# Optimization experiments

Measured on AMD Instinct MI355X. Metric: run time of the kernel, lower is better.

## Reference

```python
import jax, jax.numpy as jnp
import numpy as np

N_NODES = 100000
N_EDGES = 640000
NIN = 128
NOUT = 128


def setup_inputs() -> dict:
    key = jax.random.key(0)
    ks = jax.random.split(key, 10)
    scale = 1.0 / np.sqrt(NIN)
    x = jax.random.normal(ks[0], (N_NODES, NIN), dtype=jnp.float32)
    edge_index = jax.random.randint(ks[1], (2, N_EDGES), 0, N_NODES, dtype=jnp.int64)
    edge_attr = jnp.zeros((N_EDGES, 1), dtype=jnp.float32)
    Wk = jax.random.uniform(ks[2], (NIN, NOUT), jnp.float32, -scale, scale)
    bk = jax.random.uniform(ks[3], (NOUT,), jnp.float32, -scale, scale)
    Wq = jax.random.uniform(ks[4], (NIN, NOUT), jnp.float32, -scale, scale)
    bq = jax.random.uniform(ks[5], (NOUT,), jnp.float32, -scale, scale)
    Wv = jax.random.uniform(ks[6], (NIN, NOUT), jnp.float32, -scale, scale)
    bv = jax.random.uniform(ks[7], (NOUT,), jnp.float32, -scale, scale)
    Wskip = jax.random.uniform(ks[8], (NIN, NOUT), jnp.float32, -scale, scale)
    bias = jax.random.uniform(ks[9], (NOUT,), jnp.float32, -scale, scale)
    return {
        "x": x, "edge_index": edge_index, "edge_attr": edge_attr,
        "Wk": Wk, "bk": bk, "Wq": Wq, "bq": bq,
        "Wv": Wv, "bv": bv, "Wskip": Wskip, "bias": bias,
    }


def reference(x, edge_index, edge_attr, Wk, bk, Wq, bq, Wv, bv, Wskip, bias):
    # PyG ResGatedGraphConv: out_i = W_skip x_i + b + sum_{j->i} sigmoid(k_i + q_j) * v_j
    # k = lin_key(x) (applied to dst), q = lin_query(x) (src), v = lin_value(x) (src)
    src, dst = edge_index[0], edge_index[1]
    k = x @ Wk + bk            # [N, NOUT]
    q = x @ Wq + bq            # [N, NOUT]
    v = x @ Wv + bv            # [N, NOUT]
    eta = jax.nn.sigmoid(k[dst] + q[src])   # [E, NOUT] per-edge gate
    msg = eta * v[src]                       # [E, NOUT]
    agg = jax.ops.segment_sum(msg, dst, num_segments=x.shape[0])  # [N, NOUT]
    return agg + x @ Wskip + bias
```

## Files before the change

kernel.cpp:

```cpp
#include <hip/hip_runtime.h>
#include <hip/hip_bf16.h>

typedef __bf16 v4bf __attribute__((ext_vector_type(4)));
typedef __bf16 v8bf __attribute__((ext_vector_type(8)));
typedef float  v16f __attribute__((ext_vector_type(16)));
typedef float  f4v  __attribute__((ext_vector_type(4)));
typedef unsigned int u4v __attribute__((ext_vector_type(4)));

#define LOG2E 1.44269504088896340736f

__device__ __forceinline__ unsigned short f2bf(float f) {
    union { float f; unsigned int u; } a; a.f = f;
    unsigned int r = a.u + 0x7FFFu + ((a.u >> 16) & 1u);
    return (unsigned short)(r >> 16);
}

__device__ __forceinline__ void unpack8v(u4v w, float* f) {
    #pragma unroll
    for (int i = 0; i < 4; ++i) {
        f[2 * i]     = __uint_as_float(w[i] << 16);
        f[2 * i + 1] = __uint_as_float(w[i] & 0xFFFF0000u);
    }
}

__global__ __launch_bounds__(256) void prep_w_zero(
    const float* __restrict__ Wk, const float* __restrict__ Wq,
    const float* __restrict__ Wv, const float* __restrict__ Ws,
    unsigned short* __restrict__ Wt, int* __restrict__ deg, int N)
{
    int i = blockIdx.x * 256 + threadIdx.x;
    if (i < 65536) {
        int m = i >> 14;
        int r = i & 16383;
        int n = r >> 7, k = r & 127;
        const float* W = (m == 0) ? Wk : (m == 1) ? Wq : (m == 2) ? Wv : Ws;
        float scale = (m == 0) ? -LOG2E : (m == 1) ? LOG2E : 1.0f;
        Wt[i] = f2bf(W[k * 128 + n] * scale);
    }
    if (i < N) deg[i] = 0;
}

__global__ __launch_bounds__(1024, 4) void gemm_fused(
    const float* __restrict__ x, int N,
    const unsigned short* __restrict__ Wt,
    const float* __restrict__ bk, const float* __restrict__ bq,
    const float* __restrict__ bv, const float* __restrict__ bs,
    unsigned short* __restrict__ kws, unsigned short* __restrict__ qv,
    float* __restrict__ out,
    const int* __restrict__ ei, int E,
    int* __restrict__ deg, int* __restrict__ pos)
{
    for (int e = blockIdx.x * 1024 + threadIdx.x; e < E; e += 1024 * 1024) {
        pos[e] = atomicAdd(&deg[ei[E + e]], 1);
    }

    __shared__ __align__(16) unsigned short xs[32 * 132];
    const int t   = threadIdx.x;
    const int wid = t >> 6;
    const int m   = wid >> 2;
    const int ct  = wid & 3;
    const int l   = t & 63;
    const int col = ct * 32 + (l & 31);
    const int kb  = (l >> 5) * 8;

    v8bf b[8];
    {
        const unsigned short* wp = Wt + m * 16384 + col * 128 + kb;
        #pragma unroll
        for (int c = 0; c < 8; ++c) b[c] = *(const v8bf*)(wp + c * 16);
    }
    const float* bvec = (m == 0) ? bk : (m == 1) ? bq : (m == 2) ? bv : bs;
    const float bcol = bvec[col] * ((m == 0) ? -LOG2E : (m == 1) ? LOG2E : 1.0f);
    unsigned short* dst; int dstride;
    if (m == 0)      { dst = kws;      dstride = 128; }
    else if (m == 1) { dst = qv;       dstride = 256; }
    else             { dst = qv + 128; dstride = 256; }

    const int srow = t >> 5;
    const int sk4  = (t & 31) << 2;
    const int rowb = 4 * (l >> 5);

    const int ntiles = (N + 31) >> 5;
    int tile = blockIdx.x;
    if (tile >= ntiles) return;

    float4 stg = make_float4(0.f, 0.f, 0.f, 0.f);
    {
        int gr = tile * 32 + srow;
        if (gr < N) stg = *(const float4*)(x + (size_t)gr * 128 + sk4);
    }

    const unsigned short* ap = xs + (l & 31) * 132 + kb;

    while (true) {
        ushort4 pk;
        pk.x = f2bf(stg.x); pk.y = f2bf(stg.y);
        pk.z = f2bf(stg.z); pk.w = f2bf(stg.w);
        *(ushort4*)(xs + srow * 132 + sk4) = pk;
        __syncthreads();

        int next = tile + gridDim.x;
        if (next < ntiles) {
            int gr = next * 32 + srow;
            stg = (gr < N) ? *(const float4*)(x + (size_t)gr * 128 + sk4)
                           : make_float4(0.f, 0.f, 0.f, 0.f);
        }

        v16f acc = {};
        #pragma unroll
        for (int c = 0; c < 8; ++c) {
            v4bf a0 = *(const v4bf*)(ap + c * 16);
            v4bf a1 = *(const v4bf*)(ap + c * 16 + 4);
            v8bf a = __builtin_shufflevector(a0, a1, 0, 1, 2, 3, 4, 5, 6, 7);
            acc = __builtin_amdgcn_mfma_f32_32x32x16_bf16(a, b[c], acc, 0, 0, 0);
        }

        const int r0 = tile * 32 + rowb;
        if (m == 3) {
            #pragma unroll
            for (int reg = 0; reg < 16; ++reg) {
                int row = r0 + (reg & 3) + 8 * (reg >> 2);
                if (row < N) out[(size_t)row * 128 + col] = acc[reg] + bcol;
            }
        } else {
            #pragma unroll
            for (int reg = 0; reg < 16; ++reg) {
                int row = r0 + (reg & 3) + 8 * (reg >> 2);
                if (row < N) dst[(size_t)row * dstride + col] = f2bf(acc[reg] + bcol);
            }
        }

        tile = next;
        if (tile >= ntiles) break;
        __syncthreads();
    }
}


__global__ __launch_bounds__(256) void scan_chunks(
    const int* __restrict__ deg, int N, int* __restrict__ rowStart,
    int* __restrict__ chunkTot)
{
    __shared__ int sums[256];
    const int t = threadIdx.x;
    const int base = blockIdx.x * 1024 + t * 4;
    int d0 = 0, d1 = 0, d2 = 0, d3 = 0;
    if (base + 3 < N) {
        int4 dd = *(const int4*)(deg + base);
        d0 = dd.x; d1 = dd.y; d2 = dd.z; d3 = dd.w;
    } else {
        if (base + 0 < N) d0 = deg[base + 0];
        if (base + 1 < N) d1 = deg[base + 1];
        if (base + 2 < N) d2 = deg[base + 2];
        if (base + 3 < N) d3 = deg[base + 3];
    }
    int tot = d0 + d1 + d2 + d3;
    sums[t] = tot;
    __syncthreads();
    #pragma unroll
    for (int off = 1; off < 256; off <<= 1) {
        int v = (t >= off) ? sums[t - off] : 0;
        __syncthreads();
        sums[t] += v;
        __syncthreads();
    }
    int excl = sums[t] - tot;
    if (base + 0 < N) rowStart[base + 0] = excl;
    if (base + 1 < N) rowStart[base + 1] = excl + d0;
    if (base + 2 < N) rowStart[base + 2] = excl + d0 + d1;
    if (base + 3 < N) rowStart[base + 3] = excl + d0 + d1 + d2;
    if (t == 255) chunkTot[blockIdx.x] = sums[255];
}

__global__ __launch_bounds__(256) void add_offsets(
    int* __restrict__ rowStart, const int* __restrict__ chunkTot,
    int N, int nChunks)
{
    __shared__ int s[128];
    const int t = threadIdx.x;
    if (t < 128) s[t] = (t < nChunks) ? chunkTot[t] : 0;
    __syncthreads();
    #pragma unroll
    for (int off = 1; off < 128; off <<= 1) {
        int u = 0;
        if (t < 128 && t >= off) u = s[t - off];
        __syncthreads();
        if (t < 128) s[t] += u;
        __syncthreads();
    }
    const int coff = (blockIdx.x == 0) ? 0 : s[blockIdx.x - 1];
    const int base = blockIdx.x * 1024 + t * 4;
    if (base + 3 < N) {
        int4 r = *(const int4*)(rowStart + base);
        r.x += coff; r.y += coff; r.z += coff; r.w += coff;
        *(int4*)(rowStart + base) = r;
    } else {
        #pragma unroll
        for (int j = 0; j < 4; ++j) {
            if (base + j < N) rowStart[base + j] += coff;
        }
    }
}

__global__ __launch_bounds__(256) void fill_csr(
    const int* __restrict__ ei, int E,
    const int* __restrict__ rowStart, const int* __restrict__ pos,
    int* __restrict__ elist)
{
    int e = blockIdx.x * 256 + threadIdx.x;
    if (e >= E) return;
    elist[rowStart[ei[E + e]] + pos[e]] = ei[e];
}

__global__ __launch_bounds__(256, 4) void gather_agg(
    const int* __restrict__ rowStart, const int* __restrict__ deg,
    const int* __restrict__ elist,
    const unsigned short* __restrict__ kws,
    const unsigned short* __restrict__ qv,
    float* __restrict__ out, int N)
{
    const int grp = threadIdx.x >> 4;
    const int fo  = (threadIdx.x & 15) << 3;
    const int gstride = gridDim.x * 16;
    const unsigned short* qvb = qv + fo;

    for (int node = blockIdx.x * 16 + grp; node < N; node += gstride) {
        float* orow = out + (size_t)node * 128 + fo;
        f4v o0 = *(const f4v*)(orow);
        f4v o1 = *(const f4v*)(orow + 4);
        u4v kraw = *(const u4v*)(kws + (size_t)node * 128 + fo);
        const int p0 = rowStart[node];
        const int dg = deg[node];
        const int e  = p0 + dg;
        const int eL = e - 1;

        float nkf[8];
        unpack8v(kraw, nkf);
        float acc[8] = {};

        for (int base = p0; base < e; base += 4) {
            int idx[4];
            #pragma unroll
            for (int s = 0; s < 4; ++s) {
                int pp = base + s;
                idx[s] = elist[pp < e ? pp : eL];
            }
            u4v qr[4], vr[4];
            #pragma unroll
            for (int s = 0; s < 4; ++s) {
                const unsigned short* r = qvb + (idx[s] << 8);
                qr[s] = *(const u4v*)(r);
                vr[s] = *(const u4v*)(r + 128);
            }
            #pragma unroll
            for (int s = 0; s < 4; ++s) {
                u4v vv = vr[s];
                if (base + s >= e) { vv[0] = 0u; vv[1] = 0u; vv[2] = 0u; vv[3] = 0u; }
                float qf[8], vf[8];
                unpack8v(qr[s], qf);
                unpack8v(vv, vf);
                #pragma unroll
                for (int j = 0; j < 8; ++j) {
                    float ex = __builtin_amdgcn_exp2f(nkf[j] - qf[j]);
                    acc[j] = fmaf(__builtin_amdgcn_rcpf(1.0f + ex), vf[j], acc[j]);
                }
            }
        }

        o0[0] += acc[0]; o0[1] += acc[1]; o0[2] += acc[2]; o0[3] += acc[3];
        o1[0] += acc[4]; o1[1] += acc[5]; o1[2] += acc[6]; o1[3] += acc[7];
        *(f4v*)(orow)     = o0;
        *(f4v*)(orow + 4) = o1;
    }
}

extern "C" void kernel_launch(void* const* d_in, const int* in_sizes, int n_in,
                              void* d_out, int out_size, void* d_ws, size_t ws_size,
                              hipStream_t stream) {
    const float* x    = (const float*)d_in[0];
    const int*   ei   = (const int*)d_in[1];
    const float* Wk   = (const float*)d_in[3];
    const float* bk   = (const float*)d_in[4];
    const float* Wq   = (const float*)d_in[5];
    const float* bq   = (const float*)d_in[6];
    const float* Wv   = (const float*)d_in[7];
    const float* bv   = (const float*)d_in[8];
    const float* Ws   = (const float*)d_in[9];
    const float* bias = (const float*)d_in[10];

    const int N = in_sizes[0] / 128;
    const int E = in_sizes[1] / 2;
    float* out = (float*)d_out;

    unsigned short* kws = (unsigned short*)d_ws;
    unsigned short* qv  = kws + (size_t)N * 128;
    int* deg      = (int*)(qv + (size_t)N * 256);
    int* rowStart = deg + N;
    int* chunkTot = rowStart + N;
    int* pos      = chunkTot + 128;
    int* elist    = pos + E;
    unsigned short* Wt = (unsigned short*)(elist + E);

    const int nChunks = (N + 1023) / 1024;

    prep_w_zero<<<512, 256, 0, stream>>>(Wk, Wq, Wv, Ws, Wt, deg, N);
    gemm_fused<<<1024, 1024, 0, stream>>>(
        x, N, Wt, bk, bq, bv, bias, kws, qv, out, ei, E, deg, pos);

    scan_chunks<<<nChunks, 256, 0, stream>>>(deg, N, rowStart, chunkTot);
    add_offsets<<<nChunks, 256, 0, stream>>>(rowStart, chunkTot, N, nChunks);
    fill_csr<<<(E + 255) / 256, 256, 0, stream>>>(ei, E, rowStart, pos, elist);

    gather_agg<<<1024, 256, 0, stream>>>(
        rowStart, deg, elist, kws, qv, out, N);
}
```

Before: 260.4 us.

## Restructure fused GEMM to one 128-row tile per block with vectorized stores

The projection GEMM kernel now launches one block per 128-row tile instead of a persistent 1024-block loop over 32-row tiles. Each block stages all 128 rows of x into LDS once and reuses the register-resident weights for four MFMA row subtiles. MFMA operands are swapped so each lane holds one row's consecutive output columns, which allows float4/ushort4 row-contiguous stores instead of scattered scalar stores. Separately, the gather kernel gets a higher occupancy hint and twice as many blocks; the larger LDS tile may lower GEMM occupancy.

```diff
diff --git a/kernel.cpp b/kernel.cpp
--- a/kernel.cpp
+++ b/kernel.cpp
@@ -50,89 +50,106 @@
     const int* __restrict__ ei, int E,
     int* __restrict__ deg, int* __restrict__ pos)
 {
-    for (int e = blockIdx.x * 1024 + threadIdx.x; e < E; e += 1024 * 1024) {
+    for (int e = blockIdx.x * 1024 + threadIdx.x; e < E; e += gridDim.x * 1024) {
         pos[e] = atomicAdd(&deg[ei[E + e]], 1);
     }
 
-    __shared__ __align__(16) unsigned short xs[32 * 132];
-    const int t   = threadIdx.x;
+    __shared__ __align__(16) unsigned short xs[128 * 132];
+    const int t  = threadIdx.x;
+    const int tb = blockIdx.x * 128;
+
+    {
+        const int srow = t >> 3;
+        const int scol = (t & 7) << 4;
+        const int gr = tb + srow;
+        float4 f0, f1, f2, f3;
+        if (gr < N) {
+            const float* xp = x + (size_t)gr * 128 + scol;
+            f0 = *(const float4*)(xp);
+            f1 = *(const float4*)(xp + 4);
+            f2 = *(const float4*)(xp + 8);
+            f3 = *(const float4*)(xp + 12);
+        } else {
+            f0 = f1 = f2 = f3 = make_float4(0.f, 0.f, 0.f, 0.f);
+        }
+        unsigned short* sp = xs + srow * 132 + scol;
+        ushort4 p;
+        p.x = f2bf(f0.x); p.y = f2bf(f0.y); p.z = f2bf(f0.z); p.w = f2bf(f0.w);
+        *(ushort4*)(sp) = p;
+        p.x = f2bf(f1.x); p.y = f2bf(f1.y); p.z = f2bf(f1.z); p.w = f2bf(f1.w);
+        *(ushort4*)(sp + 4) = p;
+        p.x = f2bf(f2.x); p.y = f2bf(f2.y); p.z = f2bf(f2.z); p.w = f2bf(f2.w);
+        *(ushort4*)(sp + 8) = p;
+        p.x = f2bf(f3.x); p.y = f2bf(f3.y); p.z = f2bf(f3.z); p.w = f2bf(f3.w);
+        *(ushort4*)(sp + 12) = p;
+    }
+
     const int wid = t >> 6;
     const int m   = wid >> 2;
     const int ct  = wid & 3;
     const int l   = t & 63;
-    const int col = ct * 32 + (l & 31);
-    const int kb  = (l >> 5) * 8;
+    const int lr  = l & 31;
+    const int h   = l >> 5;
+    const int kb  = h * 8;
 
     v8bf b[8];
     {
-        const unsigned short* wp = Wt + m * 16384 + col * 128 + kb;
+        const unsigned short* wp = Wt + m * 16384 + (ct * 32 + lr) * 128 + kb;
         #pragma unroll
         for (int c = 0; c < 8; ++c) b[c] = *(const v8bf*)(wp + c * 16);
     }
     const float* bvec = (m == 0) ? bk : (m == 1) ? bq : (m == 2) ? bv : bs;
-    const float bcol = bvec[col] * ((m == 0) ? -LOG2E : (m == 1) ? LOG2E : 1.0f);
+    const float bscale = (m == 0) ? -LOG2E : (m == 1) ? LOG2E : 1.0f;
+    float4 biasg[4];
+    #pragma unroll
+    for (int g = 0; g < 4; ++g) {
+        float4 bb = *(const float4*)(bvec + ct * 32 + 8 * g + 4 * h);
+        biasg[g] = make_float4(bb.x * bscale, bb.y * bscale, bb.z * bscale, bb.w * bscale);
+    }
     unsigned short* dst; int dstride;
     if (m == 0)      { dst = kws;      dstride = 128; }
     else if (m == 1) { dst = qv;       dstride = 256; }
     else             { dst = qv + 128; dstride = 256; }
 
-    const int srow = t >> 5;
-    const int sk4  = (t & 31) << 2;
-    const int rowb = 4 * (l >> 5);
-
-    const int ntiles = (N + 31) >> 5;
-    int tile = blockIdx.x;
-    if (tile >= ntiles) return;
-
-    float4 stg = make_float4(0.f, 0.f, 0.f, 0.f);
-    {
-        int gr = tile * 32 + srow;
-        if (gr < N) stg = *(const float4*)(x + (size_t)gr * 128 + sk4);
-    }
-
-    const unsigned short* ap = xs + (l & 31) * 132 + kb;
-
-    while (true) {
-        ushort4 pk;
-        pk.x = f2bf(stg.x); pk.y = f2bf(stg.y);
-        pk.z = f2bf(stg.z); pk.w = f2bf(stg.w);
-        *(ushort4*)(xs + srow * 132 + sk4) = pk;
-        __syncthreads();
-
-        int next = tile + gridDim.x;
-        if (next < ntiles) {
-            int gr = next * 32 + srow;
-            stg = (gr < N) ? *(const float4*)(x + (size_t)gr * 128 + sk4)
-                           : make_float4(0.f, 0.f, 0.f, 0.f);
-        }
-
+    __syncthreads();
+
+    #pragma unroll
+    for (int rt = 0; rt < 4; ++rt) {
+        const unsigned short* ap = xs + (rt * 32 + lr) * 132 + kb;
         v16f acc = {};
         #pragma unroll
         for (int c = 0; c < 8; ++c) {
             v4bf a0 = *(const v4bf*)(ap + c * 16);
             v4bf a1 = *(const v4bf*)(ap + c * 16 + 4);
             v8bf a = __builtin_shufflevector(a0, a1, 0, 1, 2, 3, 4, 5, 6, 7);
-            acc = __builtin_amdgcn_mfma_f32_32x32x16_bf16(a, b[c], acc, 0, 0, 0);
-        }
-
-        const int r0 = tile * 32 + rowb;
-        if (m == 3) {
-            #pragma unroll
-            for (int reg = 0; reg < 16; ++reg) {
-                int row = r0 + (reg & 3) + 8 * (reg >> 2);
-                if (row < N) out[(size_t)row * 128 + col] = acc[reg] + bcol;
+            acc = __builtin_amdgcn_mfma_f32_32x32x16_bf16(b[c], a, acc, 0, 0, 0);
+        }
+        const int row = tb + rt * 32 + lr;
+        if (row < N) {
+            if (m == 3) {
+                float* orow = out + (size_t)row * 128 + ct * 32 + 4 * h;
+                #pragma unroll
+                for (int g = 0; g < 4; ++g) {
+                    float4 o;
+                    o.x = acc[4 * g + 0] + biasg[g].x;
+                    o.y = acc[4 * g + 1] + biasg[g].y;
+                    o.z = acc[4 * g + 2] + biasg[g].z;
+                    o.w = acc[4 * g + 3] + biasg[g].w;
+                    *(float4*)(orow + 8 * g) = o;
+                }
+            } else {
+                unsigned short* drow = dst + (size_t)row * dstride + ct * 32 + 4 * h;
+                #pragma unroll
+                for (int g = 0; g < 4; ++g) {
+                    ushort4 p;
+                    p.x = f2bf(acc[4 * g + 0] + biasg[g].x);
+                    p.y = f2bf(acc[4 * g + 1] + biasg[g].y);
+                    p.z = f2bf(acc[4 * g + 2] + biasg[g].z);
+                    p.w = f2bf(acc[4 * g + 3] + biasg[g].w);
+                    *(ushort4*)(drow + 8 * g) = p;
+                }
             }
-        } else {
-            #pragma unroll
-            for (int reg = 0; reg < 16; ++reg) {
-                int row = r0 + (reg & 3) + 8 * (reg >> 2);
-                if (row < N) dst[(size_t)row * dstride + col] = f2bf(acc[reg] + bcol);
-            }
-        }
-
-        tile = next;
-        if (tile >= ntiles) break;
-        __syncthreads();
+        }
     }
 }
 
@@ -212,7 +229,7 @@
     elist[rowStart[ei[E + e]] + pos[e]] = ei[e];
 }
 
-__global__ __launch_bounds__(256, 4) void gather_agg(
+__global__ __launch_bounds__(256, 8) void gather_agg(
     const int* __restrict__ rowStart, const int* __restrict__ deg,
     const int* __restrict__ elist,
     const unsigned short* __restrict__ kws,
@@ -302,15 +319,16 @@
     unsigned short* Wt = (unsigned short*)(elist + E);
 
     const int nChunks = (N + 1023) / 1024;
+    const int ntiles128 = (N + 127) >> 7;
 
     prep_w_zero<<<512, 256, 0, stream>>>(Wk, Wq, Wv, Ws, Wt, deg, N);
-    gemm_fused<<<1024, 1024, 0, stream>>>(
+    gemm_fused<<<ntiles128, 1024, 0, stream>>>(
         x, N, Wt, bk, bq, bv, bias, kws, qv, out, ei, E, deg, pos);
 
     scan_chunks<<<nChunks, 256, 0, stream>>>(deg, N, rowStart, chunkTot);
     add_offsets<<<nChunks, 256, 0, stream>>>(rowStart, chunkTot, N, nChunks);
     fill_csr<<<(E + 255) / 256, 256, 0, stream>>>(ei, E, rowStart, pos, elist);
 
-    gather_agg<<<1024, 256, 0, stream>>>(
+    gather_agg<<<2048, 256, 0, stream>>>(
         rowStart, deg, elist, kws, qv, out, N);
 }
```

Result: slower. 304.5 us (+16.9%).

## Restructure CSR build: fuse counting, single-pass scan, and fill into GEMM

Applied to the files above, without the earlier changes.

Moves the per-edge degree counting out of the GEMM kernel into the weight-prep kernel, replaces the two-kernel chunk scan with a single decoupled-lookback style scan using flags, and fuses the CSR fill into the GEMM kernel. The degree and flag arrays are zeroed with a memset. The gather kernel switches from a grid-stride loop to one 16-thread group per node with a full grid. The aim is fewer kernel launches and less serialization, at the cost of a spin-wait on flags across blocks, which assumes earlier blocks get scheduled first, and an extra memset launch.

```diff
diff --git a/kernel.cpp b/kernel.cpp
--- a/kernel.cpp
+++ b/kernel.cpp
@@ -23,10 +23,12 @@
     }
 }
 
-__global__ __launch_bounds__(256) void prep_w_zero(
+__global__ __launch_bounds__(256) void prep_count(
     const float* __restrict__ Wk, const float* __restrict__ Wq,
     const float* __restrict__ Wv, const float* __restrict__ Ws,
-    unsigned short* __restrict__ Wt, int* __restrict__ deg, int N)
+    unsigned short* __restrict__ Wt,
+    const int* __restrict__ ei, int E,
+    int* __restrict__ deg, int* __restrict__ pos)
 {
     int i = blockIdx.x * 256 + threadIdx.x;
     if (i < 65536) {
@@ -37,10 +39,66 @@
         float scale = (m == 0) ? -LOG2E : (m == 1) ? LOG2E : 1.0f;
         Wt[i] = f2bf(W[k * 128 + n] * scale);
     }
-    if (i < N) deg[i] = 0;
-}
-
-__global__ __launch_bounds__(1024, 4) void gemm_fused(
+    for (int e = i; e < E; e += 131072) {
+        pos[e] = atomicAdd(&deg[ei[E + e]], 1);
+    }
+}
+
+__global__ __launch_bounds__(256) void scan_fused(
+    const int* __restrict__ deg, int N, int* __restrict__ rowStart,
+    int* __restrict__ flag)
+{
+    __shared__ int sums[256];
+    __shared__ int red[256];
+    const int t = threadIdx.x;
+    const int b = blockIdx.x;
+    const int base = b * 1024 + t * 4;
+    int d0 = 0, d1 = 0, d2 = 0, d3 = 0;
+    if (base + 3 < N) {
+        int4 dd = *(const int4*)(deg + base);
+        d0 = dd.x; d1 = dd.y; d2 = dd.z; d3 = dd.w;
+    } else {
+        if (base + 0 < N) d0 = deg[base + 0];
+        if (base + 1 < N) d1 = deg[base + 1];
+        if (base + 2 < N) d2 = deg[base + 2];
+        if (base + 3 < N) d3 = deg[base + 3];
+    }
+    int tot = d0 + d1 + d2 + d3;
+    sums[t] = tot;
+    __syncthreads();
+    #pragma unroll
+    for (int off = 1; off < 256; off <<= 1) {
+        int v = (t >= off) ? sums[t - off] : 0;
+        __syncthreads();
+        sums[t] += v;
+        __syncthreads();
+    }
+    if (t == 255) {
+        __threadfence();
+        atomicExch(&flag[b], sums[255] + 1);
+    }
+    int partial = 0;
+    for (int j = t; j < b; j += 256) {
+        int v;
+        do { v = atomicAdd(&flag[j], 0); } while (v == 0);
+        partial += v - 1;
+    }
+    red[t] = partial;
+    __syncthreads();
+    #pragma unroll
+    for (int off = 128; off > 0; off >>= 1) {
+        if (t < off) red[t] += red[t + off];
+        __syncthreads();
+    }
+    const int coff = red[0];
+    int excl = sums[t] - tot + coff;
+    if (base + 0 < N) rowStart[base + 0] = excl;
+    if (base + 1 < N) rowStart[base + 1] = excl + d0;
+    if (base + 2 < N) rowStart[base + 2] = excl + d0 + d1;
+    if (base + 3 < N) rowStart[base + 3] = excl + d0 + d1 + d2;
+}
+
+__global__ __launch_bounds__(1024, 4) void gemm_fill(
     const float* __restrict__ x, int N,
     const unsigned short* __restrict__ Wt,
     const float* __restrict__ bk, const float* __restrict__ bq,
@@ -48,10 +106,11 @@
     unsigned short* __restrict__ kws, unsigned short* __restrict__ qv,
     float* __restrict__ out,
     const int* __restrict__ ei, int E,
-    int* __restrict__ deg, int* __restrict__ pos)
-{
-    for (int e = blockIdx.x * 1024 + threadIdx.x; e < E; e += 1024 * 1024) {
-        pos[e] = atomicAdd(&deg[ei[E + e]], 1);
+    const int* __restrict__ rowStart, const int* __restrict__ pos,
+    int* __restrict__ elist)
+{
+    for (int e = blockIdx.x * 1024 + threadIdx.x; e < E; e += gridDim.x * 1024) {
+        elist[rowStart[ei[E + e]] + pos[e]] = ei[e];
     }
 
     __shared__ __align__(16) unsigned short xs[32 * 132];
@@ -136,82 +195,6 @@
     }
 }
 
-
-__global__ __launch_bounds__(256) void scan_chunks(
-    const int* __restrict__ deg, int N, int* __restrict__ rowStart,
-    int* __restrict__ chunkTot)
-{
-    __shared__ int sums[256];
-    const int t = threadIdx.x;
-    const int base = blockIdx.x * 1024 + t * 4;
-    int d0 = 0, d1 = 0, d2 = 0, d3 = 0;
-    if (base + 3 < N) {
-        int4 dd = *(const int4*)(deg + base);
-        d0 = dd.x; d1 = dd.y; d2 = dd.z; d3 = dd.w;
-    } else {
-        if (base + 0 < N) d0 = deg[base + 0];
-        if (base + 1 < N) d1 = deg[base + 1];
-        if (base + 2 < N) d2 = deg[base + 2];
-        if (base + 3 < N) d3 = deg[base + 3];
-    }
-    int tot = d0 + d1 + d2 + d3;
-    sums[t] = tot;
-    __syncthreads();
-    #pragma unroll
-    for (int off = 1; off < 256; off <<= 1) {
-        int v = (t >= off) ? sums[t - off] : 0;
-        __syncthreads();
-        sums[t] += v;
-        __syncthreads();
-    }
-    int excl = sums[t] - tot;
-    if (base + 0 < N) rowStart[base + 0] = excl;
-    if (base + 1 < N) rowStart[base + 1] = excl + d0;
-    if (base + 2 < N) rowStart[base + 2] = excl + d0 + d1;
-    if (base + 3 < N) rowStart[base + 3] = excl + d0 + d1 + d2;
-    if (t == 255) chunkTot[blockIdx.x] = sums[255];
-}
-
-__global__ __launch_bounds__(256) void add_offsets(
-    int* __restrict__ rowStart, const int* __restrict__ chunkTot,
-    int N, int nChunks)
-{
-    __shared__ int s[128];
-    const int t = threadIdx.x;
-    if (t < 128) s[t] = (t < nChunks) ? chunkTot[t] : 0;
-    __syncthreads();
-    #pragma unroll
-    for (int off = 1; off < 128; off <<= 1) {
-        int u = 0;
-        if (t < 128 && t >= off) u = s[t - off];
-        __syncthreads();
-        if (t < 128) s[t] += u;
-        __syncthreads();
-    }
-    const int coff = (blockIdx.x == 0) ? 0 : s[blockIdx.x - 1];
-    const int base = blockIdx.x * 1024 + t * 4;
-    if (base + 3 < N) {
-        int4 r = *(const int4*)(rowStart + base);
-        r.x += coff; r.y += coff; r.z += coff; r.w += coff;
-        *(int4*)(rowStart + base) = r;
-    } else {
-        #pragma unroll
-        for (int j = 0; j < 4; ++j) {
-            if (base + j < N) rowStart[base + j] += coff;
-        }
-    }
-}
-
-__global__ __launch_bounds__(256) void fill_csr(
-    const int* __restrict__ ei, int E,
-    const int* __restrict__ rowStart, const int* __restrict__ pos,
-    int* __restrict__ elist)
-{
-    int e = blockIdx.x * 256 + threadIdx.x;
-    if (e >= E) return;
-    elist[rowStart[ei[E + e]] + pos[e]] = ei[e];
-}
-
 __global__ __launch_bounds__(256, 4) void gather_agg(
     const int* __restrict__ rowStart, const int* __restrict__ deg,
     const int* __restrict__ elist,
@@ -219,59 +202,59 @@
     const unsigned short* __restrict__ qv,
     float* __restrict__ out, int N)
 {
-    const int grp = threadIdx.x >> 4;
-    const int fo  = (threadIdx.x & 15) << 3;
-    const int gstride = gridDim.x * 16;
+    int gid = blockIdx.x * 256 + threadIdx.x;
+    int node = gid >> 4;
+    if (node >= N) return;
+    const int fo = (gid & 15) << 3;
+
+    float* orow = out + (size_t)node * 128 + fo;
+    f4v o0 = *(const f4v*)(orow);
+    f4v o1 = *(const f4v*)(orow + 4);
+    u4v kraw = *(const u4v*)(kws + (size_t)node * 128 + fo);
+    const int p0 = rowStart[node];
+    const int dg = deg[node];
+    const int e  = p0 + dg;
+    const int eL = e - 1;
+
+    float nkf[8];
+    unpack8v(kraw, nkf);
+    float acc[8] = {};
+
     const unsigned short* qvb = qv + fo;
 
-    for (int node = blockIdx.x * 16 + grp; node < N; node += gstride) {
-        float* orow = out + (size_t)node * 128 + fo;
-        f4v o0 = *(const f4v*)(orow);
-        f4v o1 = *(const f4v*)(orow + 4);
-        u4v kraw = *(const u4v*)(kws + (size_t)node * 128 + fo);
-        const int p0 = rowStart[node];
-        const int dg = deg[node];
-        const int e  = p0 + dg;
-        const int eL = e - 1;
-
-        float nkf[8];
-        unpack8v(kraw, nkf);
-        float acc[8] = {};
-
-        for (int base = p0; base < e; base += 4) {
-            int idx[4];
+    for (int base = p0; base < e; base += 4) {
+        int idx[4];
+        #pragma unroll
+        for (int s = 0; s < 4; ++s) {
+            int pp = base + s;
+            idx[s] = elist[pp < e ? pp : eL];
+        }
+        u4v qr[4], vr[4];
+        #pragma unroll
+        for (int s = 0; s < 4; ++s) {
+            const unsigned short* r = qvb + (idx[s] << 8);
+            qr[s] = *(const u4v*)(r);
+            vr[s] = *(const u4v*)(r + 128);
+        }
+        #pragma unroll
+        for (int s = 0; s < 4; ++s) {
+            u4v vv = vr[s];
+            if (base + s >= e) { vv[0] = 0u; vv[1] = 0u; vv[2] = 0u; vv[3] = 0u; }
+            float qf[8], vf[8];
+            unpack8v(qr[s], qf);
+            unpack8v(vv, vf);
             #pragma unroll
-            for (int s = 0; s < 4; ++s) {
-                int pp = base + s;
-                idx[s] = elist[pp < e ? pp : eL];
+            for (int j = 0; j < 8; ++j) {
+                float ex = __builtin_amdgcn_exp2f(nkf[j] - qf[j]);
+                acc[j] = fmaf(__builtin_amdgcn_rcpf(1.0f + ex), vf[j], acc[j]);
             }
-            u4v qr[4], vr[4];
-            #pragma unroll
-            for (int s = 0; s < 4; ++s) {
-                const unsigned short* r = qvb + (idx[s] << 8);
-                qr[s] = *(const u4v*)(r);
-                vr[s] = *(const u4v*)(r + 128);
-            }
-            #pragma unroll
-            for (int s = 0; s < 4; ++s) {
-                u4v vv = vr[s];
-                if (base + s >= e) { vv[0] = 0u; vv[1] = 0u; vv[2] = 0u; vv[3] = 0u; }
-                float qf[8], vf[8];
-                unpack8v(qr[s], qf);
-                unpack8v(vv, vf);
-                #pragma unroll
-                for (int j = 0; j < 8; ++j) {
-                    float ex = __builtin_amdgcn_exp2f(nkf[j] - qf[j]);
-                    acc[j] = fmaf(__builtin_amdgcn_rcpf(1.0f + ex), vf[j], acc[j]);
-                }
-            }
-        }
-
-        o0[0] += acc[0]; o0[1] += acc[1]; o0[2] += acc[2]; o0[3] += acc[3];
-        o1[0] += acc[4]; o1[1] += acc[5]; o1[2] += acc[6]; o1[3] += acc[7];
-        *(f4v*)(orow)     = o0;
-        *(f4v*)(orow + 4) = o1;
-    }
+        }
+    }
+
+    o0[0] += acc[0]; o0[1] += acc[1]; o0[2] += acc[2]; o0[3] += acc[3];
+    o1[0] += acc[4]; o1[1] += acc[5]; o1[2] += acc[6]; o1[3] += acc[7];
+    *(f4v*)(orow)     = o0;
+    *(f4v*)(orow + 4) = o1;
 }
 
 extern "C" void kernel_launch(void* const* d_in, const int* in_sizes, int n_in,
@@ -295,22 +278,20 @@
     unsigned short* kws = (unsigned short*)d_ws;
     unsigned short* qv  = kws + (size_t)N * 128;
     int* deg      = (int*)(qv + (size_t)N * 256);
-    int* rowStart = deg + N;
-    int* chunkTot = rowStart + N;
-    int* pos      = chunkTot + 128;
+    int* flag     = deg + N;
+    int* rowStart = flag + 128;
+    int* pos      = rowStart + N;
     int* elist    = pos + E;
     unsigned short* Wt = (unsigned short*)(elist + E);
 
     const int nChunks = (N + 1023) / 1024;
 
-    prep_w_zero<<<512, 256, 0, stream>>>(Wk, Wq, Wv, Ws, Wt, deg, N);
-    gemm_fused<<<1024, 1024, 0, stream>>>(
-        x, N, Wt, bk, bq, bv, bias, kws, qv, out, ei, E, deg, pos);
-
-    scan_chunks<<<nChunks, 256, 0, stream>>>(deg, N, rowStart, chunkTot);
-    add_offsets<<<nChunks, 256, 0, stream>>>(rowStart, chunkTot, N, nChunks);
-    fill_csr<<<(E + 255) / 256, 256, 0, stream>>>(ei, E, rowStart, pos, elist);
-
-    gather_agg<<<1024, 256, 0, stream>>>(
+    hipMemsetAsync(deg, 0, (size_t)(N + 128) * sizeof(int), stream);
+
+    prep_count<<<512, 256, 0, stream>>>(Wk, Wq, Wv, Ws, Wt, ei, E, deg, pos);
+    scan_fused<<<nChunks, 256, 0, stream>>>(deg, N, rowStart, flag);
+    gemm_fill<<<1024, 1024, 0, stream>>>(
+        x, N, Wt, bk, bq, bv, bias, kws, qv, out, ei, E, rowStart, pos, elist);
+    gather_agg<<<((size_t)N * 16 + 255) / 256, 256, 0, stream>>>(
         rowStart, deg, elist, kws, qv, out, N);
 }
```

New measurement: 264.1 us. No clear change (+1.4%).
